# Kernel tuning notes

Hardware: AMD Instinct MI355X
Metric: run time of the kernel (lower is better)

## Reference

```python
import jax, jax.numpy as jnp
import numpy as np

B, S, D = 2, 2048, 1024
H = 16
HD = D // H
RANK = 8
ALPHA = 8.0
NEG = -1e9


def setup_inputs() -> dict:
    key = jax.random.key(0)
    ks = jax.random.split(key, 7)
    inv = 1.0 / np.sqrt(D)
    return {
        "x": jax.random.normal(ks[0], (B, S, D), dtype=jnp.float32),
        "W_qkv": jax.random.normal(ks[1], (D, 3 * D), dtype=jnp.float32) * inv,
        "b_qkv": jax.random.normal(ks[2], (3 * D,), dtype=jnp.float32) * 0.02,
        # LoRA: A ~ N(0, 1/rank) per torch init; B is zeros at init but given
        # small values here so the LoRA path is exercised numerically.
        "A_lora": jax.random.normal(ks[3], (D, RANK), dtype=jnp.float32) / np.sqrt(RANK),
        "B_lora": jax.random.normal(ks[4], (RANK, 3 * D), dtype=jnp.float32) * 0.02,
        "W_proj": jax.random.normal(ks[5], (D, D), dtype=jnp.float32) * inv,
        "b_proj": jax.random.normal(ks[6], (D,), dtype=jnp.float32) * 0.02,
    }


def _split_heads(t):
    # [B, S, D] -> [B, H, S, HD]
    return t.reshape(B, S, H, HD).transpose(0, 2, 1, 3)


def reference(x, W_qkv, b_qkv, A_lora, B_lora, W_proj, b_proj):
    # c_attn: LoRALayer -> base linear + alpha * (x @ A @ B)
    qkv = x @ W_qkv + b_qkv + (x @ A_lora @ B_lora) * ALPHA  # [B, S, 3D]
    q, k, v = jnp.split(qkv, 3, axis=-1)
    q, k, v = _split_heads(q), _split_heads(k), _split_heads(v)

    # SelfAttentionFunction: QK^T, add mask, THEN divide by sqrt(head_dim)
    causal = jnp.tril(jnp.ones((S, S), dtype=bool))
    mask = jnp.where(causal, 0.0, NEG).astype(x.dtype)  # [S, S] additive
    scores = (jnp.einsum("bhqd,bhkd->bhqk", q, k) + mask) / jnp.sqrt(
        jnp.asarray(HD, dtype=x.dtype)
    )
    attn = jax.nn.softmax(scores, axis=-1)  # [B, H, S, S]
    ctx = jnp.einsum("bhqk,bhkd->bhqd", attn, v)  # [B, H, S, HD]

    # merge heads -> c_proj (plain LoRaLinear: x @ W + b)
    ctx = ctx.transpose(0, 2, 1, 3).reshape(B, S, D)
    out = ctx @ W_proj + b_proj
    return out
```

## Files before the change

kernel.cpp:

```cpp
#include <hip/hip_runtime.h>
#include <hip/hip_bf16.h>


#define BB    2
#define SS    2048
#define DD    1024
#define HH    16
#define HDIM  64
#define N3    3072
#define MR    4096

typedef short short8 __attribute__((ext_vector_type(8)));
typedef float f32x4 __attribute__((ext_vector_type(4)));

#define MFMA16(a, b, c) __builtin_amdgcn_mfma_f32_16x16x32_bf16((a), (b), (c), 0, 0, 0)

__device__ __forceinline__ float b2f(short s) {
    union { unsigned int u; float f; } c;
    c.u = ((unsigned int)(unsigned short)s) << 16;
    return c.f;
}
__device__ __forceinline__ short f2b(float f) {
    union { __hip_bfloat16 h; short s; } c;
    c.h = __float2bfloat16(f);
    return c.s;
}
struct HiLo { short hi, lo; };
__device__ __forceinline__ HiLo split2(float v) {
    HiLo r;
    r.hi = f2b(v);
    r.lo = f2b(v - b2f(r.hi));
    return r;
}

__device__ __forceinline__ void gl_lds16(const void* g, void* l) {
    __builtin_amdgcn_global_load_lds(
        (const __attribute__((address_space(1))) void*)g,
        (__attribute__((address_space(3))) void*)l, 16, 0, 0);
}


__global__ __launch_bounds__(256) void split_x(const float* __restrict__ X,
                                               short* __restrict__ Xhi,
                                               short* __restrict__ Xlo) {
    int kc = blockIdx.x, p = blockIdx.y;
    int tid = threadIdx.x;
    int row = tid >> 1, half = tid & 1;
    const float* src = &X[((size_t)p * 128 + row) * 1024 + kc * 32 + half * 16];
    f32x4 v[4];
#pragma unroll
    for (int u = 0; u < 4; u++) v[u] = *(const f32x4*)(src + u * 4);
    size_t base = ((size_t)p * 32 + kc) * 4096 + (size_t)(half * 2) * 1024 + row * 8;
#pragma unroll
    for (int u = 0; u < 2; u++) {
        short8 h8, l8;
#pragma unroll
        for (int j = 0; j < 8; j++) {
            HiLo hl = split2(v[u * 2 + (j >> 2)][j & 3]);
            h8[j] = hl.hi; l8[j] = hl.lo;
        }
        *(short8*)&Xhi[base + u * 1024] = h8;
        *(short8*)&Xlo[base + u * 1024] = l8;
    }
}

__global__ __launch_bounds__(256) void prep_kernel(
    const float* __restrict__ W, const float* __restrict__ Al,
    const float* __restrict__ Bl, short* __restrict__ Whi,
    short* __restrict__ Wlo, int N, int lora)
{
    __shared__ float sw[64][68];
    __shared__ float sa[64][8];
    __shared__ float sb[8][64];
    int tid = threadIdx.x;
    int n0 = blockIdx.x * 64, k0 = blockIdx.y * 64;
#pragma unroll
    for (int p = 0; p < 4; p++) {
        int idx = p * 256 + tid;
        int kr = idx >> 4, ch = idx & 15;
        *(f32x4*)&sw[kr][ch * 4] = *(const f32x4*)&W[(size_t)(k0 + kr) * N + n0 + ch * 4];
    }
    if (lora) {
        if (tid < 64) {
#pragma unroll
            for (int r = 0; r < 8; r++) sa[tid][r] = Al[(k0 + tid) * 8 + r];
        } else if (tid < 128) {
            int c = tid - 64;
#pragma unroll
            for (int r = 0; r < 8; r++) sb[r][c] = Bl[(size_t)r * N + n0 + c];
        }
    }
    __syncthreads();
#pragma unroll
    for (int p = 0; p < 2; p++) {
        int idx = p * 256 + tid;
        int nr = idx >> 3, ch = idx & 7;
        short8 h8, l8;
#pragma unroll
        for (int j = 0; j < 8; j++) {
            int k = ch * 8 + j;
            float v = sw[k][nr];
            if (lora) {
                float a2 = 0.f;
#pragma unroll
                for (int r = 0; r < 8; r++) a2 += sa[k][r] * sb[r][nr];
                v += 8.0f * a2;
            }
            HiLo hl = split2(v);
            h8[j] = hl.hi;
            l8[j] = hl.lo;
        }
        int n = n0 + nr;
        int kchunk = (k0 >> 5) + (ch >> 2);
        size_t off = ((size_t)(n >> 7) * 32 + kchunk) * 4096 +
                     (size_t)(ch & 3) * 1024 + (n & 127) * 8;
        *(short8*)&Whi[off] = h8;
        *(short8*)&Wlo[off] = l8;
    }
}

__global__ __launch_bounds__(256) void gemm3(
    const short* __restrict__ Ahi, const short* __restrict__ Alo,
    const short* __restrict__ Bhi, const short* __restrict__ Blo,
    const float* __restrict__ bias,
    float* __restrict__ qf, short* __restrict__ khi, short* __restrict__ klo,
    short* __restrict__ vt, float* __restrict__ outf32, int N, int mode)
{
    __shared__ short lds[4][4][128][8];
    int tid = threadIdx.x;
    int wav = tid >> 6, lane = tid & 63;
    int l15 = lane & 15, q4 = lane >> 4;
    int wm = wav & 1, wn = wav >> 1;
    int n0 = blockIdx.x * 128, m0 = blockIdx.y * 128;

    const short* ga_h = Ahi + ((size_t)blockIdx.y * 32) * 4096 + tid * 8;
    const short* ga_l = Alo + ((size_t)blockIdx.y * 32) * 4096 + tid * 8;
    const short* gb_h = Bhi + ((size_t)blockIdx.x * 32) * 4096 + tid * 8;
    const short* gb_l = Blo + ((size_t)blockIdx.x * 32) * 4096 + tid * 8;
    short* l0 = &lds[0][0][0][0] + tid * 8;

    f32x4 acc[4][4] = {};

    for (int kc = 0; kc < 32; ++kc) {
        __syncthreads();
        int koff = kc * 4096;
        gl_lds16(ga_h + koff,        l0);
        gl_lds16(ga_h + koff + 2048, l0 + 2048);
        gl_lds16(ga_l + koff,        l0 + 4096);
        gl_lds16(ga_l + koff + 2048, l0 + 6144);
        gl_lds16(gb_h + koff,        l0 + 8192);
        gl_lds16(gb_h + koff + 2048, l0 + 10240);
        gl_lds16(gb_l + koff,        l0 + 12288);
        gl_lds16(gb_l + koff + 2048, l0 + 14336);
        __syncthreads();
        short8 ah[4], al_[4], bh[4], bl[4];
#pragma unroll
        for (int i = 0; i < 4; i++) {
            ah[i]  = *(short8*)&lds[0][q4][wm * 64 + i * 16 + l15][0];
            al_[i] = *(short8*)&lds[1][q4][wm * 64 + i * 16 + l15][0];
            bh[i]  = *(short8*)&lds[2][q4][wn * 64 + i * 16 + l15][0];
            bl[i]  = *(short8*)&lds[3][q4][wn * 64 + i * 16 + l15][0];
        }
#pragma unroll
        for (int mi = 0; mi < 4; mi++)
#pragma unroll
            for (int ni = 0; ni < 4; ni++) {
                acc[mi][ni] = MFMA16(ah[mi], bh[ni], acc[mi][ni]);
                acc[mi][ni] = MFMA16(ah[mi], bl[ni], acc[mi][ni]);
                acc[mi][ni] = MFMA16(al_[mi], bh[ni], acc[mi][ni]);
            }
    }
#pragma unroll
    for (int ni = 0; ni < 4; ni++) {
        int n = n0 + wn * 64 + ni * 16 + l15;
        float bv = bias[n];
#pragma unroll
        for (int mi = 0; mi < 4; mi++) {
            int mbase = m0 + wm * 64 + mi * 16 + q4 * 4;
#pragma unroll
            for (int r = 0; r < 4; r++) {
                int m = mbase + r;
                float v = acc[mi][ni][r] + bv;
                if (mode != 0) {
                    outf32[(size_t)m * 1024 + n] = v;
                } else if (n0 < 1024) {
                    qf[(size_t)m * 1024 + n] = v * 0.125f;
                } else if (n0 < 2048) {
                    int kk = n - 1024, hh = kk >> 6, hd = kk & 63;
                    int bb_ = m >> 11, s = m & 2047;
                    size_t base = ((size_t)((bb_ << 4) + hh) * 32 + (s >> 6)) * 4096
                                  + (size_t)(hd >> 3) * 512 + (s & 63) * 8 + (hd & 7);
                    HiLo hl = split2(v);
                    khi[base] = hl.hi;
                    klo[base] = hl.lo;
                } else {
                    int kk = n - 2048, hh = kk >> 6, hd = kk & 63;
                    int bb_ = m >> 11, s = m & 2047;
                    size_t base = ((size_t)((bb_ << 4) + hh) * 32 + (s >> 6)) * 4096
                                  + (size_t)((s >> 3) & 7) * 512 + hd * 8 + (s & 7);
                    vt[base] = f2b(v);
                }
            }
        }
    }
}

__global__ __launch_bounds__(256) void attn_mfma(const float* __restrict__ qf,
                                                 const short* __restrict__ khi,
                                                 const short* __restrict__ klo,
                                                 const short* __restrict__ vtg,
                                                 short* __restrict__ ctxhi,
                                                 short* __restrict__ ctxlo) {
    __shared__ short KhL[2][4096];
    __shared__ short KlL[2][4096];
    __shared__ short VtL[2][4096];
    __shared__ short Pt[4][8][17][8];

    int h = blockIdx.y, b = blockIdx.z;
    int tid = threadIdx.x, wav = tid >> 6, lane = tid & 63;
    int l15 = lane & 15, q4 = lane >> 4;
    const float* bq = qf + (size_t)b * SS * 1024;
    size_t hb = (size_t)((b * 16 + h) * 32) * 4096;
    const short* gkh = khi + hb;
    const short* gkl = klo + hb;
    const short* gvt = vtg + hb;
    int t8 = tid * 8;

#define ISSUE(c, buf)                                                   \
    {                                                                   \
        size_t co_ = (size_t)(c) * 4096 + t8;                           \
        gl_lds16(gkh + co_,        &KhL[buf][t8]);                      \
        gl_lds16(gkh + co_ + 2048, &KhL[buf][t8 + 2048]);               \
        gl_lds16(gkl + co_,        &KlL[buf][t8]);                      \
        gl_lds16(gkl + co_ + 2048, &KlL[buf][t8 + 2048]);               \
        gl_lds16(gvt + co_,        &VtL[buf][t8]);                      \
        gl_lds16(gvt + co_ + 2048, &VtL[buf][t8 + 2048]);               \
    }

    for (int t = 0; t < 2; ++t) {
        int qt = t ? (int)blockIdx.x : 31 - (int)blockIdx.x;
        int qb = qt * 64;

        size_t qoff = (size_t)(qb + wav * 16 + l15) * 1024 + h * 64;
        short8 q0h, q0l, q1h, q1l;
        {
            f32x4 a0 = *(const f32x4*)&bq[qoff + q4 * 8];
            f32x4 a1 = *(const f32x4*)&bq[qoff + q4 * 8 + 4];
            f32x4 c0 = *(const f32x4*)&bq[qoff + 32 + q4 * 8];
            f32x4 c1 = *(const f32x4*)&bq[qoff + 32 + q4 * 8 + 4];
#pragma unroll
            for (int j = 0; j < 4; j++) {
                HiLo u = split2(a0[j]); q0h[j] = u.hi; q0l[j] = u.lo;
                HiLo v = split2(a1[j]); q0h[4 + j] = v.hi; q0l[4 + j] = v.lo;
                HiLo w = split2(c0[j]); q1h[j] = w.hi; q1l[j] = w.lo;
                HiLo z = split2(c1[j]); q1h[4 + j] = z.hi; q1l[4 + j] = z.lo;
            }
        }

        f32x4 o[4] = {};
        float m[4]  = {-1e30f, -1e30f, -1e30f, -1e30f};
        float lsum[4] = {0.f, 0.f, 0.f, 0.f};
        int nch = qt + 1;

        ISSUE(0, 0);
        __syncthreads();

        for (int c = 0; c < nch; ++c) {
            int cur = c & 1;
            int k0 = c * 64;

            if (c + 1 < nch) ISSUE(c + 1, cur ^ 1);

            f32x4 s[4];
#pragma unroll
            for (int g = 0; g < 4; g++) {
                int ko = (g * 16 + l15) * 8;
                short8 k0h_ = *(short8*)&KhL[cur][q4 * 512 + ko];
                short8 k0l_ = *(short8*)&KlL[cur][q4 * 512 + ko];
                short8 k1h_ = *(short8*)&KhL[cur][(4 + q4) * 512 + ko];
                short8 k1l_ = *(short8*)&KlL[cur][(4 + q4) * 512 + ko];
                f32x4 acc = {};
                acc = MFMA16(q0h, k0h_, acc);
                acc = MFMA16(q0h, k0l_, acc);
                acc = MFMA16(q0l, k0h_, acc);
                acc = MFMA16(q1h, k1h_, acc);
                acc = MFMA16(q1h, k1l_, acc);
                acc = MFMA16(q1l, k1h_, acc);
                s[g] = acc;
            }

            float alpha[4];
#pragma unroll
            for (int r = 0; r < 4; r++) {
                float a[4];
#pragma unroll
                for (int g = 0; g < 4; g++) a[g] = s[g][r];
                if (c == qt) {
                    int q = qb + wav * 16 + q4 * 4 + r;
#pragma unroll
                    for (int g = 0; g < 4; g++) {
                        int key = k0 + g * 16 + l15;
                        if (key > q) a[g] = -1e30f;
                    }
                }
                float mx = fmaxf(fmaxf(a[0], a[1]), fmaxf(a[2], a[3]));
                mx = fmaxf(mx, __shfl_xor(mx, 1, 64));
                mx = fmaxf(mx, __shfl_xor(mx, 2, 64));
                mx = fmaxf(mx, __shfl_xor(mx, 4, 64));
                mx = fmaxf(mx, __shfl_xor(mx, 8, 64));
                float mn = fmaxf(m[r], mx);
                float p0 = __expf(a[0] - mn), p1 = __expf(a[1] - mn);
                float p2 = __expf(a[2] - mn), p3 = __expf(a[3] - mn);
                float sm = p0 + p1 + p2 + p3;
                sm += __shfl_xor(sm, 1, 64);
                sm += __shfl_xor(sm, 2, 64);
                sm += __shfl_xor(sm, 4, 64);
                sm += __shfl_xor(sm, 8, 64);
                alpha[r] = __expf(m[r] - mn);
                m[r] = mn;
                lsum[r] = lsum[r] * alpha[r] + sm;
                int kq = (l15 >> 3), j = l15 & 7, row = q4 * 4 + r;
                Pt[wav][0 + kq][row][j] = f2b(p0);
                Pt[wav][2 + kq][row][j] = f2b(p1);
                Pt[wav][4 + kq][row][j] = f2b(p2);
                Pt[wav][6 + kq][row][j] = f2b(p3);
            }

            short8 pf0 = *(short8*)&Pt[wav][q4][l15][0];
            short8 pf1 = *(short8*)&Pt[wav][4 + q4][l15][0];
#pragma unroll
            for (int gg = 0; gg < 4; gg++) {
                int vo = (gg * 16 + l15) * 8;
                short8 vf0 = *(short8*)&VtL[cur][q4 * 512 + vo];
                short8 vf1 = *(short8*)&VtL[cur][(4 + q4) * 512 + vo];
                f32x4 tt = o[gg];
                tt[0] *= alpha[0]; tt[1] *= alpha[1]; tt[2] *= alpha[2]; tt[3] *= alpha[3];
                tt = MFMA16(pf0, vf0, tt);
                tt = MFMA16(pf1, vf1, tt);
                o[gg] = tt;
            }

            __syncthreads();
        }

#pragma unroll
        for (int gg = 0; gg < 4; gg++)
#pragma unroll
            for (int r = 0; r < 4; r++) {
                int q = qb + wav * 16 + q4 * 4 + r;
                int mrow = b * SS + q;
                int k = h * 64 + gg * 16 + l15;
                HiLo hl = split2(o[gg][r] / lsum[r]);
                size_t off = ((size_t)(mrow >> 7) * 32 + (k >> 5)) * 4096 +
                             (size_t)((k >> 3) & 3) * 1024 + (mrow & 127) * 8 + (k & 7);
                ctxhi[off] = hl.hi;
                ctxlo[off] = hl.lo;
            }
    }
#undef ISSUE
}

extern "C" void kernel_launch(void* const* d_in, const int* in_sizes, int n_in,
                              void* d_out, int out_size, void* d_ws, size_t ws_size,
                              hipStream_t stream) {
    const float* x  = (const float*)d_in[0];
    const float* Wq = (const float*)d_in[1];
    const float* bq = (const float*)d_in[2];
    const float* Al = (const float*)d_in[3];
    const float* Bl = (const float*)d_in[4];
    const float* Wp = (const float*)d_in[5];
    const float* bp = (const float*)d_in[6];

    char* ws = (char*)d_ws;
    float* qf     = (float*)(ws);
    short* khi    = (short*)(ws + (size_t)16 * 1024 * 1024);
    short* klo    = (short*)(ws + (size_t)24 * 1024 * 1024);
    short* vt     = (short*)(ws + (size_t)32 * 1024 * 1024);
    short* wpt_hi = (short*)(ws + (size_t)40 * 1024 * 1024);
    short* wpt_lo = (short*)(ws + (size_t)42 * 1024 * 1024);
    short* wqt_hi = (short*)(ws + (size_t)44 * 1024 * 1024);
    short* wqt_lo = (short*)(ws + (size_t)50 * 1024 * 1024);
    short* xhi    = (short*)(ws + (size_t)56 * 1024 * 1024);
    short* xlo    = (short*)(ws + (size_t)64 * 1024 * 1024);
    short* ctxhi  = (short*)(ws + (size_t)44 * 1024 * 1024);
    short* ctxlo  = (short*)(ws + (size_t)52 * 1024 * 1024);

    hipLaunchKernelGGL(split_x, dim3(32, 32), dim3(256), 0, stream, x, xhi, xlo);
    hipLaunchKernelGGL(prep_kernel, dim3(N3 / 64, 16), dim3(256), 0, stream,
                       Wq, Al, Bl, wqt_hi, wqt_lo, N3, 1);
    hipLaunchKernelGGL(prep_kernel, dim3(DD / 64, 16), dim3(256), 0, stream,
                       Wp, (const float*)nullptr, (const float*)nullptr,
                       wpt_hi, wpt_lo, DD, 0);
    hipLaunchKernelGGL(gemm3, dim3(N3 / 128, MR / 128), dim3(256), 0, stream,
                       xhi, xlo, wqt_hi, wqt_lo, bq,
                       qf, khi, klo, vt, (float*)nullptr, N3, 0);
    hipLaunchKernelGGL(attn_mfma, dim3(SS / 128, HH, BB), dim3(256), 0, stream,
                       qf, khi, klo, vt, ctxhi, ctxlo);
    hipLaunchKernelGGL(gemm3, dim3(DD / 128, MR / 128), dim3(256), 0, stream,
                       ctxhi, ctxlo, wpt_hi, wpt_lo, bp,
                       (float*)nullptr, (short*)nullptr, (short*)nullptr,
                       (short*)nullptr, (float*)d_out, DD, 1);
}
```

Measured before the change: 319.9 us.

## Swizzle K/V LDS layout, transpose QK^T MFMA, and simplify softmax reductions

The K and V^T tiles are written to global memory in an XOR-swizzled layout, and the LDS reads use the matching addresses, to avoid shared-memory bank conflicts. The QK^T MFMA operands are swapped so each lane holds one query row's scores. That cuts the per-row max and sum reductions to two cross-lane shuffles and lets P be stored as packed 4-element vectors. It also adds s_setprio around the MFMA blocks, at the cost of extra shuffles to redistribute alpha and the row sums back to the output layout.

```diff
diff --git a/kernel.cpp b/kernel.cpp
--- a/kernel.cpp
+++ b/kernel.cpp
@@ -11,6 +11,7 @@
 #define MR    4096
 
 typedef short short8 __attribute__((ext_vector_type(8)));
+typedef short s16x4 __attribute__((ext_vector_type(4)));
 typedef float f32x4 __attribute__((ext_vector_type(4)));
 
 #define MFMA16(a, b, c) __builtin_amdgcn_mfma_f32_16x16x32_bf16((a), (b), (c), 0, 0, 0)
@@ -188,16 +189,18 @@
                 } else if (n0 < 2048) {
                     int kk = n - 1024, hh = kk >> 6, hd = kk & 63;
                     int bb_ = m >> 11, s = m & 2047;
+                    int oct = hd >> 3;
                     size_t base = ((size_t)((bb_ << 4) + hh) * 32 + (s >> 6)) * 4096
-                                  + (size_t)(hd >> 3) * 512 + (s & 63) * 8 + (hd & 7);
+                                  + (size_t)oct * 512 + ((s & 63) ^ oct) * 8 + (hd & 7);
                     HiLo hl = split2(v);
                     khi[base] = hl.hi;
                     klo[base] = hl.lo;
                 } else {
                     int kk = n - 2048, hh = kk >> 6, hd = kk & 63;
                     int bb_ = m >> 11, s = m & 2047;
+                    int oct = (s >> 3) & 7;
                     size_t base = ((size_t)((bb_ << 4) + hh) * 32 + (s >> 6)) * 4096
-                                  + (size_t)((s >> 3) & 7) * 512 + hd * 8 + (s & 7);
+                                  + (size_t)oct * 512 + (hd ^ oct) * 8 + (s & 7);
                     vt[base] = f2b(v);
                 }
             }
@@ -258,8 +261,8 @@
         }
 
         f32x4 o[4] = {};
-        float m[4]  = {-1e30f, -1e30f, -1e30f, -1e30f};
-        float lsum[4] = {0.f, 0.f, 0.f, 0.f};
+        float msc = -1e30f;
+        float lsc = 0.f;
         int nch = qt + 1;
 
         ISSUE(0, 0);
@@ -272,77 +275,92 @@
             if (c + 1 < nch) ISSUE(c + 1, cur ^ 1);
 
             f32x4 s[4];
+            __builtin_amdgcn_s_setprio(1);
 #pragma unroll
             for (int g = 0; g < 4; g++) {
-                int ko = (g * 16 + l15) * 8;
-                short8 k0h_ = *(short8*)&KhL[cur][q4 * 512 + ko];
-                short8 k0l_ = *(short8*)&KlL[cur][q4 * 512 + ko];
-                short8 k1h_ = *(short8*)&KhL[cur][(4 + q4) * 512 + ko];
-                short8 k1l_ = *(short8*)&KlL[cur][(4 + q4) * 512 + ko];
+                int ko  = q4 * 512 + ((g * 16 + l15) ^ q4) * 8;
+                int ko2 = (4 + q4) * 512 + ((g * 16 + l15) ^ (4 + q4)) * 8;
+                short8 k0h_ = *(short8*)&KhL[cur][ko];
+                short8 k0l_ = *(short8*)&KlL[cur][ko];
+                short8 k1h_ = *(short8*)&KhL[cur][ko2];
+                short8 k1l_ = *(short8*)&KlL[cur][ko2];
                 f32x4 acc = {};
-                acc = MFMA16(q0h, k0h_, acc);
-                acc = MFMA16(q0h, k0l_, acc);
-                acc = MFMA16(q0l, k0h_, acc);
-                acc = MFMA16(q1h, k1h_, acc);
-                acc = MFMA16(q1h, k1l_, acc);
-                acc = MFMA16(q1l, k1h_, acc);
+                acc = MFMA16(k0h_, q0h, acc);
+                acc = MFMA16(k0l_, q0h, acc);
+                acc = MFMA16(k0h_, q0l, acc);
+                acc = MFMA16(k1h_, q1h, acc);
+                acc = MFMA16(k1l_, q1h, acc);
+                acc = MFMA16(k1h_, q1l, acc);
                 s[g] = acc;
             }
-
-            float alpha[4];
-#pragma unroll
-            for (int r = 0; r < 4; r++) {
-                float a[4];
-#pragma unroll
-                for (int g = 0; g < 4; g++) a[g] = s[g][r];
-                if (c == qt) {
-                    int q = qb + wav * 16 + q4 * 4 + r;
-#pragma unroll
-                    for (int g = 0; g < 4; g++) {
-                        int key = k0 + g * 16 + l15;
-                        if (key > q) a[g] = -1e30f;
-                    }
+            __builtin_amdgcn_s_setprio(0);
+
+            if (c == qt) {
+                int q = qb + wav * 16 + l15;
+#pragma unroll
+                for (int g = 0; g < 4; g++)
+#pragma unroll
+                    for (int r = 0; r < 4; r++)
+                        if (k0 + g * 16 + q4 * 4 + r > q) s[g][r] = -1e30f;
+            }
+            f32x4 mx4 = s[0];
+#pragma unroll
+            for (int g = 1; g < 4; g++) {
+                mx4[0] = fmaxf(mx4[0], s[g][0]); mx4[1] = fmaxf(mx4[1], s[g][1]);
+                mx4[2] = fmaxf(mx4[2], s[g][2]); mx4[3] = fmaxf(mx4[3], s[g][3]);
+            }
+            float mx = fmaxf(fmaxf(mx4[0], mx4[1]), fmaxf(mx4[2], mx4[3]));
+            mx = fmaxf(mx, __shfl_xor(mx, 16, 64));
+            mx = fmaxf(mx, __shfl_xor(mx, 32, 64));
+            float mn = fmaxf(msc, mx);
+            f32x4 ps = {};
+#pragma unroll
+            for (int g = 0; g < 4; g++) {
+                s16x4 pb;
+#pragma unroll
+                for (int r = 0; r < 4; r++) {
+                    float p = __expf(s[g][r] - mn);
+                    ps[r] += p;
+                    pb[r] = f2b(p);
                 }
-                float mx = fmaxf(fmaxf(a[0], a[1]), fmaxf(a[2], a[3]));
-                mx = fmaxf(mx, __shfl_xor(mx, 1, 64));
-                mx = fmaxf(mx, __shfl_xor(mx, 2, 64));
-                mx = fmaxf(mx, __shfl_xor(mx, 4, 64));
-                mx = fmaxf(mx, __shfl_xor(mx, 8, 64));
-                float mn = fmaxf(m[r], mx);
-                float p0 = __expf(a[0] - mn), p1 = __expf(a[1] - mn);
-                float p2 = __expf(a[2] - mn), p3 = __expf(a[3] - mn);
-                float sm = p0 + p1 + p2 + p3;
-                sm += __shfl_xor(sm, 1, 64);
-                sm += __shfl_xor(sm, 2, 64);
-                sm += __shfl_xor(sm, 4, 64);
-                sm += __shfl_xor(sm, 8, 64);
-                alpha[r] = __expf(m[r] - mn);
-                m[r] = mn;
-                lsum[r] = lsum[r] * alpha[r] + sm;
-                int kq = (l15 >> 3), j = l15 & 7, row = q4 * 4 + r;
-                Pt[wav][0 + kq][row][j] = f2b(p0);
-                Pt[wav][2 + kq][row][j] = f2b(p1);
-                Pt[wav][4 + kq][row][j] = f2b(p2);
-                Pt[wav][6 + kq][row][j] = f2b(p3);
-            }
+                *(s16x4*)&Pt[wav][g * 2 + (q4 >> 1)][l15][(q4 & 1) * 4] = pb;
+            }
+            float sm = (ps[0] + ps[1]) + (ps[2] + ps[3]);
+            sm += __shfl_xor(sm, 16, 64);
+            sm += __shfl_xor(sm, 32, 64);
+            float alpha_s = __expf(msc - mn);
+            msc = mn;
+            lsc = lsc * alpha_s + sm;
+            float al0 = __shfl(alpha_s, q4 * 4 + 0, 64);
+            float al1 = __shfl(alpha_s, q4 * 4 + 1, 64);
+            float al2 = __shfl(alpha_s, q4 * 4 + 2, 64);
+            float al3 = __shfl(alpha_s, q4 * 4 + 3, 64);
 
             short8 pf0 = *(short8*)&Pt[wav][q4][l15][0];
             short8 pf1 = *(short8*)&Pt[wav][4 + q4][l15][0];
+            __builtin_amdgcn_s_setprio(1);
 #pragma unroll
             for (int gg = 0; gg < 4; gg++) {
-                int vo = (gg * 16 + l15) * 8;
-                short8 vf0 = *(short8*)&VtL[cur][q4 * 512 + vo];
-                short8 vf1 = *(short8*)&VtL[cur][(4 + q4) * 512 + vo];
+                int vo  = q4 * 512 + ((gg * 16 + l15) ^ q4) * 8;
+                int vo2 = (4 + q4) * 512 + ((gg * 16 + l15) ^ (4 + q4)) * 8;
+                short8 vf0 = *(short8*)&VtL[cur][vo];
+                short8 vf1 = *(short8*)&VtL[cur][vo2];
                 f32x4 tt = o[gg];
-                tt[0] *= alpha[0]; tt[1] *= alpha[1]; tt[2] *= alpha[2]; tt[3] *= alpha[3];
+                tt[0] *= al0; tt[1] *= al1; tt[2] *= al2; tt[3] *= al3;
                 tt = MFMA16(pf0, vf0, tt);
                 tt = MFMA16(pf1, vf1, tt);
                 o[gg] = tt;
             }
+            __builtin_amdgcn_s_setprio(0);
 
             __syncthreads();
         }
 
+        float ls0 = __shfl(lsc, q4 * 4 + 0, 64);
+        float ls1 = __shfl(lsc, q4 * 4 + 1, 64);
+        float ls2 = __shfl(lsc, q4 * 4 + 2, 64);
+        float ls3 = __shfl(lsc, q4 * 4 + 3, 64);
+        float lsr[4] = {ls0, ls1, ls2, ls3};
 #pragma unroll
         for (int gg = 0; gg < 4; gg++)
 #pragma unroll
@@ -350,7 +368,7 @@
                 int q = qb + wav * 16 + q4 * 4 + r;
                 int mrow = b * SS + q;
                 int k = h * 64 + gg * 16 + l15;
-                HiLo hl = split2(o[gg][r] / lsum[r]);
+                HiLo hl = split2(o[gg][r] / lsr[r]);
                 size_t off = ((size_t)(mrow >> 7) * 32 + (k >> 5)) * 4096 +
                              (size_t)((k >> 3) & 3) * 1024 + (mrow & 127) * 8 + (k & 7);
                 ctxhi[off] = hl.hi;
```

New measurement: 300.4 us. -6.1%, faster.
